# Kernel optimization log

Hardware: AMD Instinct MI355X
Metric: run time of the kernel (lower is better)

Reference implementation:

```python
import jax, jax.numpy as jnp
import numpy as np

B, V, D = 32768, 2, 512   # batch, views (code hard-codes 2 via cat(subject, subject)), hidden dim
S, L = 32, 8              # number of subjects, number of labels -> K = S*L groups
DENS_TEMP = 0.1           # args.Intersubsim_dens_temp (temperature/base_temperature are unused in forward)


def setup_inputs() -> dict:
    key = jax.random.key(0)
    k1, k2, k3 = jax.random.split(key, 3)
    X_data = jax.random.normal(k1, (B, V, D), dtype=jnp.float32)
    subject = jax.random.randint(k2, (B,), 0, S, dtype=jnp.int32)
    labels = jax.random.randint(k3, (B,), 0, L, dtype=jnp.int32)
    return {"X_data": X_data, "subject": subject, "labels": labels}


def reference(X_data, subject, labels):
    K = S * L
    # contrast_feature = cat(unbind(X_data, dim=1), dim=0): view-major stacking -> [V*B, D]
    feat = jnp.concatenate([X_data[:, v, :] for v in range(V)], axis=0)
    sub2 = jnp.concatenate([subject, subject])   # subject_ten
    lab2 = jnp.concatenate([labels, labels])     # labels_ten

    # group id per row; loop order (sorted unique subject, sorted unique label) == s*L + l
    gid = sub2 * L + lab2                         # [2B]
    counts = jax.ops.segment_sum(jnp.ones(gid.shape, feat.dtype), gid, K)   # [K]
    sums = jax.ops.segment_sum(feat, gid, K)                                 # [K, D]
    centroid = sums / counts[:, None]                                        # per-group mean

    # per-point euclidean distance to own-group centroid (torch.cdist)
    dist = jnp.sqrt(jnp.sum((feat - centroid[gid]) ** 2, axis=1))            # [2B]
    # density: mean(dist ** 0.5) / log(n_g + 10) for groups with >1 member
    mean_sqrt = jax.ops.segment_sum(jnp.sqrt(dist), gid, K) / counts
    dens = mean_sqrt / jnp.log(counts + 10.0)
    dmax = jnp.max(jnp.where(counts > 1, dens, -jnp.inf))
    density = jnp.where(counts > 1, dens, dmax)
    density = jnp.clip(density, jnp.quantile(density, 0.1), jnp.quantile(density, 0.9))
    density = DENS_TEMP * density / density.mean()
    # torch path goes through .tolist() -> density carries no gradient
    density = jax.lax.stop_gradient(density)

    # masks: positives = same label, different subject (group index equals raw id here)
    g_sub = jnp.arange(K, dtype=sub2.dtype) // L
    g_lab = jnp.arange(K, dtype=lab2.dtype) % L
    mask = ((sub2[:, None] != g_sub[None, :]) & (lab2[:, None] == g_lab[None, :])).astype(feat.dtype)  # [2B, K]
    # with S>=2 and all labels present, every row has at least one positive -> no row drop

    sim = (feat @ centroid.T) / density[None, :]          # [2B, K]
    sim = sim - jnp.max(sim, axis=1, keepdims=True)
    positive_sim = sim * mask
    # CrossEntropyLoss with soft (unnormalized) float targets: -sum target*log_softmax
    logp = jax.nn.log_softmax(positive_sim, axis=1)
    loss = -jnp.sum(mask * logp, axis=1) / jnp.sum(mask, axis=1)
    return loss.mean()
```

## Files before the change

### kernel.cpp

```cpp
#include <hip/hip_runtime.h>
#include <math.h>

#define BN 32768
#define DN 512
#define SN 32
#define LN 8
#define KN 256
#define N2 65536
#define SPLIT 8

typedef __attribute__((ext_vector_type(8))) short bf16x8;
typedef __attribute__((ext_vector_type(4))) float f32x4;

#define OFF_XBF     0ull
#define OFF_PART    67108864ull
#define OFF_CENTB   71303168ull
#define OFF_PERM    71827456ull
#define OFF_BASE    71958528ull
#define OFF_OFFW    71959556ull
#define OFF_COUNTS  71960580ull
#define OFF_SUMQ    71961604ull
#define OFF_INVD    71962628ull
#define OFF_LOSS    71963652ull
#define OFF_BARS    71963656ull
#define ZERO_OFF    OFF_OFFW
#define ZERO_BYTES  (71963680ull - OFF_OFFW)

__device__ __forceinline__ float atomAddF(float* p, float v) {
  return unsafeAtomicAdd(p, v);
}

__device__ __forceinline__ void gridbar_relaxed(unsigned* cnt, unsigned* flag,
                                                unsigned nblocks) {
  asm volatile("s_waitcnt vmcnt(0)" ::: "memory");
  __syncthreads();
  if (threadIdx.x == 0) {
    unsigned a = __hip_atomic_fetch_add(cnt, 1u, __ATOMIC_RELAXED,
                                        __HIP_MEMORY_SCOPE_AGENT);
    if (a + 1u == nblocks) {
      __hip_atomic_store(flag, 1u, __ATOMIC_RELAXED, __HIP_MEMORY_SCOPE_AGENT);
    } else {
      while (!__hip_atomic_load(flag, __ATOMIC_RELAXED, __HIP_MEMORY_SCOPE_AGENT))
        __builtin_amdgcn_s_sleep(16);
    }
  }
  __syncthreads();
}

__device__ __forceinline__ ushort f2bf(float x) {
  union { float f; unsigned u; } v; v.f = x;
  unsigned u = v.u;
  unsigned r = (u + 0x7fffu + ((u >> 16) & 1u)) >> 16;
  return (ushort)r;
}

__device__ __forceinline__ float bf2f(ushort x) {
  union { unsigned u; float f; } v; v.u = ((unsigned)x) << 16;
  return v.f;
}

__device__ __forceinline__ void async16(const void* g, void* l) {
  __builtin_amdgcn_global_load_lds(
      (const __attribute__((address_space(1))) unsigned int*)g,
      (__attribute__((address_space(3))) unsigned int*)l, 16, 0, 0);
}

__global__ __launch_bounds__(256) void k0_all(const int* __restrict__ subject,
    const int* __restrict__ labels, int* __restrict__ counts, int* __restrict__ base,
    int* __restrict__ offw, int* __restrict__ perm, unsigned* __restrict__ bars) {
  __shared__ int lhist[KN];
  __shared__ int sh[KN];
  __shared__ int lbase[KN];
  const int t = threadIdx.x;
  const int b0 = blockIdx.x * 1024;
  lhist[t] = 0;
  __syncthreads();
  int g[4], lr[4];
#pragma unroll
  for (int k = 0; k < 4; ++k) {
    const int b = b0 + k * 256 + t;
    g[k] = subject[b] * LN + labels[b];
    lr[k] = atomicAdd(&lhist[g[k]], 1);
  }
  __syncthreads();
  const int h = lhist[t];
  if (h) atomicAdd(&counts[t], 2 * h);
  gridbar_relaxed(&bars[0], &bars[1], 32);
  const int rows = ((int)__hip_atomic_load((unsigned*)&counts[t], __ATOMIC_RELAXED,
                                           __HIP_MEMORY_SCOPE_AGENT)) >> 1;
  sh[t] = rows;
  __syncthreads();
  for (int d = 1; d < 256; d <<= 1) {
    int add = (t >= d) ? sh[t - d] : 0;
    __syncthreads();
    sh[t] += add;
    __syncthreads();
  }
  const int excl = sh[t] - rows;
  if (blockIdx.x == 0) {
    base[t] = excl;
    if (t == 255) base[256] = sh[255];
  }
  if (h) lbase[t] = excl + atomicAdd(&offw[t], h);
  __syncthreads();
#pragma unroll
  for (int k = 0; k < 4; ++k)
    perm[lbase[g[k]] + lr[k]] = b0 + k * 256 + t;
}

__global__ __launch_bounds__(256) void k1_sums(const float* __restrict__ X,
    const int* __restrict__ perm, const int* __restrict__ base,
    ushort* __restrict__ Xb, float* __restrict__ partial) {
  __shared__ float buf[4 * 512];
  const int g = blockIdx.x >> 3;
  const int s = blockIdx.x & (SPLIT - 1);
  const int t = threadIdx.x;
  const int w = t >> 6;
  const int lane = t & 63;
  const int start = base[g], end = base[g + 1];
  const int vs = s * 4 + w;

  float4 a0 = {0.f, 0.f, 0.f, 0.f};
  float4 a1 = {0.f, 0.f, 0.f, 0.f};

  int i = start + vs;
  if (i < end) {
    int idx = perm[i];
    const float* bp = X + (size_t)idx * 1024 + lane * 4;
    float4 x0 = *(const float4*)(bp);
    float4 x1 = *(const float4*)(bp + 256);
    float4 x2 = *(const float4*)(bp + 512);
    float4 x3 = *(const float4*)(bp + 768);
    while (true) {
      const int inext = i + 32;
      int idxn = idx;
      float4 y0 = x0, y1 = x1, y2 = x2, y3 = x3;
      if (inext < end) {
        idxn = perm[inext];
        const float* bn = X + (size_t)idxn * 1024 + lane * 4;
        y0 = *(const float4*)(bn);
        y1 = *(const float4*)(bn + 256);
        y2 = *(const float4*)(bn + 512);
        y3 = *(const float4*)(bn + 768);
      }
      a0.x += x0.x + x2.x; a0.y += x0.y + x2.y;
      a0.z += x0.z + x2.z; a0.w += x0.w + x2.w;
      a1.x += x1.x + x3.x; a1.y += x1.y + x3.y;
      a1.z += x1.z + x3.z; a1.w += x1.w + x3.w;
      ushort* xb0 = Xb + (size_t)idx * DN + lane * 4;
      ushort* xb1 = Xb + (size_t)(idx + BN) * DN + lane * 4;
      *(ushort4*)(xb0)       = (ushort4){f2bf(x0.x), f2bf(x0.y), f2bf(x0.z), f2bf(x0.w)};
      *(ushort4*)(xb0 + 256) = (ushort4){f2bf(x1.x), f2bf(x1.y), f2bf(x1.z), f2bf(x1.w)};
      *(ushort4*)(xb1)       = (ushort4){f2bf(x2.x), f2bf(x2.y), f2bf(x2.z), f2bf(x2.w)};
      *(ushort4*)(xb1 + 256) = (ushort4){f2bf(x3.x), f2bf(x3.y), f2bf(x3.z), f2bf(x3.w)};
      if (inext >= end) break;
      i = inext; idx = idxn; x0 = y0; x1 = y1; x2 = y2; x3 = y3;
    }
  }
  *(float4*)&buf[w * 512 + lane * 4] = a0;
  *(float4*)&buf[w * 512 + 256 + lane * 4] = a1;
  __syncthreads();
  if (t < 128) {
    float4 r = {0.f, 0.f, 0.f, 0.f};
#pragma unroll
    for (int ww = 0; ww < 4; ++ww) {
      float4 v = *(float4*)&buf[ww * 512 + t * 4];
      r.x += v.x; r.y += v.y; r.z += v.z; r.w += v.w;
    }
    *(float4*)&partial[((size_t)s * KN + g) * DN + t * 4] = r;
  }
}

__global__ __launch_bounds__(256) void k1b_cent(const float* __restrict__ partial,
    const int* __restrict__ counts, ushort* __restrict__ centB) {
  const int i = blockIdx.x * 256 + threadIdx.x;
  const int g = i >> 9;
  float ss = 0.f;
#pragma unroll
  for (int s = 0; s < SPLIT; ++s) ss += partial[(size_t)s * (KN * DN) + i];
  centB[i] = f2bf(ss / (float)counts[g]);
}

__global__ __launch_bounds__(256) void k3_dist(const ushort* __restrict__ Xb,
    const int* __restrict__ perm, const int* __restrict__ base,
    const ushort* __restrict__ centB, const int* __restrict__ counts,
    float* __restrict__ sumq, float* __restrict__ invd,
    unsigned* __restrict__ bars) {
  __shared__ float wacc[4];
  __shared__ unsigned elect;
  __shared__ float sv[256];
  __shared__ float stv[256];
  const int g = blockIdx.x >> 3;
  const int s = blockIdx.x & (SPLIT - 1);
  const int t = threadIdx.x;
  const int w = t >> 6;
  const int lane = t & 63;
  const int start = base[g], end = base[g + 1];
  const int nviews = 2 * (end - start);
  const ushort* cp = centB + g * DN + lane * 8;
  float cs[8];
#pragma unroll
  for (int k = 0; k < 8; ++k) cs[k] = bf2f(cp[k]);
  float q = 0.f;
  const int vs = s * 4 + w;
  for (int j = vs; j < nviews; j += SPLIT * 4) {
    const int idx = perm[start + (j >> 1)];
    const int row = idx + (j & 1) * BN;
    int4 chunk = *(const int4*)(Xb + (size_t)row * DN + lane * 8);
    const ushort* us = (const ushort*)&chunk;
    float ss = 0.f;
#pragma unroll
    for (int k = 0; k < 8; ++k) {
      float diff = bf2f(us[k]) - cs[k];
      ss += diff * diff;
    }
#pragma unroll
    for (int off = 32; off > 0; off >>= 1) ss += __shfl_down(ss, off, 64);
    if (lane == 0) q += sqrtf(sqrtf(ss));
  }
  if (lane == 0) wacc[w] = q;
  __syncthreads();
  if (t == 0) atomAddF(&sumq[g], wacc[0] + wacc[1] + wacc[2] + wacc[3]);

  asm volatile("s_waitcnt vmcnt(0)" ::: "memory");
  __syncthreads();
  if (t == 0) {
    unsigned a = __hip_atomic_fetch_add(&bars[2], 1u, __ATOMIC_RELAXED,
                                        __HIP_MEMORY_SCOPE_AGENT);
    elect = (a + 1u == (unsigned)(KN * SPLIT)) ? 1u : 0u;
  }
  __syncthreads();
  if (!elect) return;

  const int cnt = counts[t];
  const bool valid = cnt > 1;
  const float sq = __hip_atomic_load(&sumq[t], __ATOMIC_RELAXED,
                                     __HIP_MEMORY_SCOPE_AGENT);
  float dens = 0.f;
  if (valid) dens = (sq / (float)cnt) / logf((float)cnt + 10.f);
  sv[t] = valid ? dens : -INFINITY;
  __syncthreads();
  for (int s2 = 128; s2 > 0; s2 >>= 1) {
    if (t < s2) sv[t] = fmaxf(sv[t], sv[t + s2]);
    __syncthreads();
  }
  const float dmax = sv[0];
  __syncthreads();
  const float d0 = valid ? dens : dmax;
  sv[t] = d0;
  __syncthreads();
  int rank = 0;
  for (int j = 0; j < 256; ++j) {
    float vj = sv[j];
    rank += (vj < d0) || (vj == d0 && j < t);
  }
  stv[rank] = d0;
  __syncthreads();
  const float q10 = 0.5f * (stv[25] + stv[26]);
  const float q90 = 0.5f * (stv[229] + stv[230]);
  const float dc = fminf(fmaxf(d0, q10), q90);
  sv[t] = dc;
  __syncthreads();
  for (int s2 = 128; s2 > 0; s2 >>= 1) {
    if (t < s2) sv[t] += sv[t + s2];
    __syncthreads();
  }
  invd[t] = (sv[0] * (1.0f / 256.f)) / (0.1f * dc);
}

#define TAB (128 * 128)
#define TBB (256 * 128)
__global__ __launch_bounds__(256, 2) void k5_mfma(const ushort* __restrict__ Xb,
    const ushort* __restrict__ centB, const int* __restrict__ subject,
    const int* __restrict__ labels, const float* __restrict__ invd,
    float* __restrict__ losssum, float* __restrict__ out,
    unsigned* __restrict__ bars) {
  __shared__ char smem[TAB + TBB + 1024];
  char* ldsA = smem;
  char* ldsB = smem + TAB;
  float* maxbuf = (float*)smem;
  float* gmax = (float*)(smem + 2048);
  float* ebuf = (float*)(smem + 2560);
  float* zbuf = (float*)(smem + 4608);
  int* labs = (int*)(smem + TAB + TBB);
  int* subs = labs + 128;

  const int t = threadIdx.x;
  const int w = t >> 6;
  const int lane = t & 63;
  const int quad = lane >> 4;
  const int n16 = lane & 15;
  const int li = lane >> 3;
  const int lc = lane & 7;
  const int srcc = lc ^ li;
  const int rowbase = blockIdx.x * 128;

  if (t < 128) {
    int b = (rowbase + t) & (BN - 1);
    labs[t] = labels[b];
    subs[t] = subject[b];
  }

  f32x4 acc[8][4];
#pragma unroll
  for (int mt = 0; mt < 8; ++mt)
#pragma unroll
    for (int nt = 0; nt < 4; ++nt) acc[mt][nt] = (f32x4){0.f, 0.f, 0.f, 0.f};

  const ushort* Arow = Xb + (size_t)rowbase * DN;

  for (int k0 = 0; k0 < DN; k0 += 64) {
    __syncthreads();
#pragma unroll
    for (int q = 0; q < 4; ++q) {
      const int r0 = w * 32 + q * 8;
      async16(Arow + (size_t)(r0 + li) * DN + k0 + srcc * 8, ldsA + r0 * 128);
    }
#pragma unroll
    for (int q = 0; q < 8; ++q) {
      const int g0 = w * 64 + q * 8;
      async16(centB + (size_t)(g0 + li) * DN + k0 + srcc * 8, ldsB + g0 * 128);
    }
    __syncthreads();
#pragma unroll
    for (int s = 0; s < 2; ++s) {
      const int csw = ((s * 4 + quad) ^ (n16 & 7)) * 16;
      bf16x8 bfr[4];
#pragma unroll
      for (int nt = 0; nt < 4; ++nt) {
        int g = w * 64 + nt * 16 + n16;
        bfr[nt] = *(bf16x8*)(ldsB + g * 128 + csw);
      }
#pragma unroll
      for (int mt = 0; mt < 8; ++mt) {
        bf16x8 afr = *(bf16x8*)(ldsA + (mt * 16 + n16) * 128 + csw);
#pragma unroll
        for (int nt = 0; nt < 4; ++nt)
          acc[mt][nt] = __builtin_amdgcn_mfma_f32_16x16x32_bf16(afr, bfr[nt], acc[mt][nt], 0, 0, 0);
      }
    }
  }

  float iv[4];
#pragma unroll
  for (int nt = 0; nt < 4; ++nt) iv[nt] = invd[w * 64 + nt * 16 + n16];

  __syncthreads();

#pragma unroll
  for (int mt = 0; mt < 8; ++mt) {
#pragma unroll
    for (int r = 0; r < 4; ++r) {
      float mm = -INFINITY;
#pragma unroll
      for (int nt = 0; nt < 4; ++nt) mm = fmaxf(mm, acc[mt][nt][r] * iv[nt]);
#pragma unroll
      for (int off = 1; off < 16; off <<= 1) mm = fmaxf(mm, __shfl_xor(mm, off, 64));
      if (n16 == 0) maxbuf[w * 128 + mt * 16 + quad * 4 + r] = mm;
    }
  }
  __syncthreads();
  if (t < 128)
    gmax[t] = fmaxf(fmaxf(maxbuf[t], maxbuf[128 + t]),
                    fmaxf(maxbuf[256 + t], maxbuf[384 + t]));
  __syncthreads();

#pragma unroll
  for (int mt = 0; mt < 8; ++mt) {
#pragma unroll
    for (int r = 0; r < 4; ++r) {
      const int row = mt * 16 + quad * 4 + r;
      const float gm = gmax[row];
      const int lab = labs[row];
      const int sub = subs[row];
      float e = 0.f, z = 0.f;
      if ((n16 & 7) == lab) {
#pragma unroll
        for (int nt = 0; nt < 4; ++nt) {
          int gdiv8 = w * 8 + nt * 2 + (n16 >> 3);
          if (gdiv8 != sub) {
            float svv = acc[mt][nt][r] * iv[nt] - gm;
            e += expf(svv);
            z += svv;
          }
        }
      }
#pragma unroll
      for (int off = 1; off < 16; off <<= 1) {
        e += __shfl_xor(e, off, 64);
        z += __shfl_xor(z, off, 64);
      }
      if (n16 == 0) {
        ebuf[w * 128 + row] = e;
        zbuf[w * 128 + row] = z;
      }
    }
  }
  __syncthreads();

  float lsum = 0.f;
  if (t < 128) {
    float e = ebuf[t] + ebuf[128 + t] + ebuf[256 + t] + ebuf[384 + t];
    float z = zbuf[t] + zbuf[128 + t] + zbuf[256 + t] + zbuf[384 + t];
    lsum = logf(225.f + e) - z * (1.0f / 31.0f);
  }
#pragma unroll
  for (int off = 32; off > 0; off >>= 1) lsum += __shfl_down(lsum, off, 64);
  if (lane == 0 && lsum != 0.f) atomAddF(losssum, lsum);

  asm volatile("s_waitcnt vmcnt(0)" ::: "memory");
  __syncthreads();
  if (t == 0) {
    unsigned a = __hip_atomic_fetch_add(&bars[4], 1u, __ATOMIC_RELAXED,
                                        __HIP_MEMORY_SCOPE_AGENT);
    if (a + 1u == (unsigned)(N2 / 128)) {
      const float ls = __hip_atomic_load(losssum, __ATOMIC_RELAXED,
                                         __HIP_MEMORY_SCOPE_AGENT);
      out[0] = ls * (1.0f / (float)N2);
    }
  }
}

extern "C" void kernel_launch(void* const* d_in, const int* in_sizes, int n_in,
                              void* d_out, int out_size, void* d_ws, size_t ws_size,
                              hipStream_t stream) {
  const float* X = (const float*)d_in[0];
  const int* subject = (const int*)d_in[1];
  const int* labels = (const int*)d_in[2];
  char* ws = (char*)d_ws;
  ushort* Xb = (ushort*)(ws + OFF_XBF);
  float* partial = (float*)(ws + OFF_PART);
  ushort* centB = (ushort*)(ws + OFF_CENTB);
  int* perm = (int*)(ws + OFF_PERM);
  int* basep = (int*)(ws + OFF_BASE);
  int* offw = (int*)(ws + OFF_OFFW);
  int* counts = (int*)(ws + OFF_COUNTS);
  float* sumq = (float*)(ws + OFF_SUMQ);
  float* invd = (float*)(ws + OFF_INVD);
  float* losssum = (float*)(ws + OFF_LOSS);
  unsigned* bars = (unsigned*)(ws + OFF_BARS);

  hipMemsetAsync(ws + ZERO_OFF, 0, ZERO_BYTES, stream);
  k0_all<<<32, 256, 0, stream>>>(subject, labels, counts, basep, offw, perm, bars);
  k1_sums<<<KN * SPLIT, 256, 0, stream>>>(X, perm, basep, Xb, partial);
  k1b_cent<<<(KN * DN) / 256, 256, 0, stream>>>(partial, counts, centB);
  k3_dist<<<KN * SPLIT, 256, 0, stream>>>(Xb, perm, basep, centB, counts,
                                          sumq, invd, bars);
  k5_mfma<<<N2 / 128, 256, 0, stream>>>(Xb, centB, subject, labels, invd,
                                        losssum, (float*)d_out, bars);
}
```

Before: 314.6 us.

## Fuse centroid finalize into distance kernel, widen bf16 stores, halve MFMA row tile

Removes the separate centroid-finalize kernel. Each distance block now reduces the split partial sums for its group into shared memory, and split 0 writes the bf16 centroid. The sums kernel now loads 8 contiguous floats per lane and writes 16-byte bf16 stores instead of 8-byte ones. The MFMA loss kernel uses 64-row tiles with launch bounds of 3 blocks per CU, giving twice as many blocks. The trade-off is redundant partial reads across the 8 split blocks and halved reuse of the centroid tile per block.

```diff
diff --git a/kernel.cpp b/kernel.cpp
--- a/kernel.cpp
+++ b/kernel.cpp
@@ -11,6 +11,7 @@
 
 typedef __attribute__((ext_vector_type(8))) short bf16x8;
 typedef __attribute__((ext_vector_type(4))) float f32x4;
+typedef __attribute__((ext_vector_type(8))) unsigned short ushort8v;
 
 #define OFF_XBF     0ull
 #define OFF_PART    67108864ull
@@ -126,39 +127,40 @@
   int i = start + vs;
   if (i < end) {
     int idx = perm[i];
-    const float* bp = X + (size_t)idx * 1024 + lane * 4;
-    float4 x0 = *(const float4*)(bp);
-    float4 x1 = *(const float4*)(bp + 256);
-    float4 x2 = *(const float4*)(bp + 512);
-    float4 x3 = *(const float4*)(bp + 768);
+    const float* bp = X + (size_t)idx * 1024 + lane * 8;
+    float4 x0  = *(const float4*)(bp);
+    float4 x0b = *(const float4*)(bp + 4);
+    float4 x1  = *(const float4*)(bp + 512);
+    float4 x1b = *(const float4*)(bp + 516);
     while (true) {
       const int inext = i + 32;
       int idxn = idx;
-      float4 y0 = x0, y1 = x1, y2 = x2, y3 = x3;
+      float4 y0 = x0, y0b = x0b, y1 = x1, y1b = x1b;
       if (inext < end) {
         idxn = perm[inext];
-        const float* bn = X + (size_t)idxn * 1024 + lane * 4;
-        y0 = *(const float4*)(bn);
-        y1 = *(const float4*)(bn + 256);
-        y2 = *(const float4*)(bn + 512);
-        y3 = *(const float4*)(bn + 768);
-      }
-      a0.x += x0.x + x2.x; a0.y += x0.y + x2.y;
-      a0.z += x0.z + x2.z; a0.w += x0.w + x2.w;
-      a1.x += x1.x + x3.x; a1.y += x1.y + x3.y;
-      a1.z += x1.z + x3.z; a1.w += x1.w + x3.w;
-      ushort* xb0 = Xb + (size_t)idx * DN + lane * 4;
-      ushort* xb1 = Xb + (size_t)(idx + BN) * DN + lane * 4;
-      *(ushort4*)(xb0)       = (ushort4){f2bf(x0.x), f2bf(x0.y), f2bf(x0.z), f2bf(x0.w)};
-      *(ushort4*)(xb0 + 256) = (ushort4){f2bf(x1.x), f2bf(x1.y), f2bf(x1.z), f2bf(x1.w)};
-      *(ushort4*)(xb1)       = (ushort4){f2bf(x2.x), f2bf(x2.y), f2bf(x2.z), f2bf(x2.w)};
-      *(ushort4*)(xb1 + 256) = (ushort4){f2bf(x3.x), f2bf(x3.y), f2bf(x3.z), f2bf(x3.w)};
+        const float* bn = X + (size_t)idxn * 1024 + lane * 8;
+        y0  = *(const float4*)(bn);
+        y0b = *(const float4*)(bn + 4);
+        y1  = *(const float4*)(bn + 512);
+        y1b = *(const float4*)(bn + 516);
+      }
+      a0.x += x0.x + x1.x;  a0.y += x0.y + x1.y;
+      a0.z += x0.z + x1.z;  a0.w += x0.w + x1.w;
+      a1.x += x0b.x + x1b.x; a1.y += x0b.y + x1b.y;
+      a1.z += x0b.z + x1b.z; a1.w += x0b.w + x1b.w;
+      ushort8v u0, u1;
+      u0[0] = f2bf(x0.x);  u0[1] = f2bf(x0.y);  u0[2] = f2bf(x0.z);  u0[3] = f2bf(x0.w);
+      u0[4] = f2bf(x0b.x); u0[5] = f2bf(x0b.y); u0[6] = f2bf(x0b.z); u0[7] = f2bf(x0b.w);
+      u1[0] = f2bf(x1.x);  u1[1] = f2bf(x1.y);  u1[2] = f2bf(x1.z);  u1[3] = f2bf(x1.w);
+      u1[4] = f2bf(x1b.x); u1[5] = f2bf(x1b.y); u1[6] = f2bf(x1b.z); u1[7] = f2bf(x1b.w);
+      *(ushort8v*)(Xb + (size_t)idx * DN + lane * 8) = u0;
+      *(ushort8v*)(Xb + (size_t)(idx + BN) * DN + lane * 8) = u1;
       if (inext >= end) break;
-      i = inext; idx = idxn; x0 = y0; x1 = y1; x2 = y2; x3 = y3;
-    }
-  }
-  *(float4*)&buf[w * 512 + lane * 4] = a0;
-  *(float4*)&buf[w * 512 + 256 + lane * 4] = a1;
+      i = inext; idx = idxn; x0 = y0; x0b = y0b; x1 = y1; x1b = y1b;
+    }
+  }
+  *(float4*)&buf[w * 512 + lane * 8] = a0;
+  *(float4*)&buf[w * 512 + lane * 8 + 4] = a1;
   __syncthreads();
   if (t < 128) {
     float4 r = {0.f, 0.f, 0.f, 0.f};
@@ -171,21 +173,12 @@
   }
 }
 
-__global__ __launch_bounds__(256) void k1b_cent(const float* __restrict__ partial,
-    const int* __restrict__ counts, ushort* __restrict__ centB) {
-  const int i = blockIdx.x * 256 + threadIdx.x;
-  const int g = i >> 9;
-  float ss = 0.f;
-#pragma unroll
-  for (int s = 0; s < SPLIT; ++s) ss += partial[(size_t)s * (KN * DN) + i];
-  centB[i] = f2bf(ss / (float)counts[g]);
-}
-
 __global__ __launch_bounds__(256) void k3_dist(const ushort* __restrict__ Xb,
     const int* __restrict__ perm, const int* __restrict__ base,
-    const ushort* __restrict__ centB, const int* __restrict__ counts,
-    float* __restrict__ sumq, float* __restrict__ invd,
-    unsigned* __restrict__ bars) {
+    const float* __restrict__ partial, const int* __restrict__ counts,
+    ushort* __restrict__ centB, float* __restrict__ sumq,
+    float* __restrict__ invd, unsigned* __restrict__ bars) {
+  __shared__ float cent[DN];
   __shared__ float wacc[4];
   __shared__ unsigned elect;
   __shared__ float sv[256];
@@ -197,10 +190,26 @@
   const int lane = t & 63;
   const int start = base[g], end = base[g + 1];
   const int nviews = 2 * (end - start);
-  const ushort* cp = centB + g * DN + lane * 8;
+  const int cnt = counts[g];
+  const float invc = 1.0f / (float)cnt;
+
+  float c0 = 0.f, c1 = 0.f;
+#pragma unroll
+  for (int sp = 0; sp < SPLIT; ++sp) {
+    float2 v = *(const float2*)&partial[(size_t)sp * (KN * DN) + g * DN + t * 2];
+    c0 += v.x; c1 += v.y;
+  }
+  c0 *= invc; c1 *= invc;
+  cent[t * 2] = c0; cent[t * 2 + 1] = c1;
+  if (s == 0) {
+    *(ushort2*)&centB[g * DN + t * 2] = (ushort2){f2bf(c0), f2bf(c1)};
+  }
+  __syncthreads();
+
   float cs[8];
 #pragma unroll
-  for (int k = 0; k < 8; ++k) cs[k] = bf2f(cp[k]);
+  for (int k = 0; k < 8; ++k) cs[k] = cent[lane * 8 + k];
+
   float q = 0.f;
   const int vs = s * 4 + w;
   for (int j = vs; j < nviews; j += SPLIT * 4) {
@@ -232,12 +241,12 @@
   __syncthreads();
   if (!elect) return;
 
-  const int cnt = counts[t];
-  const bool valid = cnt > 1;
+  const int cntt = counts[t];
+  const bool valid = cntt > 1;
   const float sq = __hip_atomic_load(&sumq[t], __ATOMIC_RELAXED,
                                      __HIP_MEMORY_SCOPE_AGENT);
   float dens = 0.f;
-  if (valid) dens = (sq / (float)cnt) / logf((float)cnt + 10.f);
+  if (valid) dens = (sq / (float)cntt) / logf((float)cntt + 10.f);
   sv[t] = valid ? dens : -INFINITY;
   __syncthreads();
   for (int s2 = 128; s2 > 0; s2 >>= 1) {
@@ -268,9 +277,9 @@
   invd[t] = (sv[0] * (1.0f / 256.f)) / (0.1f * dc);
 }
 
-#define TAB (128 * 128)
+#define TAB (64 * 128)
 #define TBB (256 * 128)
-__global__ __launch_bounds__(256, 2) void k5_mfma(const ushort* __restrict__ Xb,
+__global__ __launch_bounds__(256, 3) void k5_mfma(const ushort* __restrict__ Xb,
     const ushort* __restrict__ centB, const int* __restrict__ subject,
     const int* __restrict__ labels, const float* __restrict__ invd,
     float* __restrict__ losssum, float* __restrict__ out,
@@ -283,7 +292,7 @@
   float* ebuf = (float*)(smem + 2560);
   float* zbuf = (float*)(smem + 4608);
   int* labs = (int*)(smem + TAB + TBB);
-  int* subs = labs + 128;
+  int* subs = labs + 64;
 
   const int t = threadIdx.x;
   const int w = t >> 6;
@@ -293,17 +302,17 @@
   const int li = lane >> 3;
   const int lc = lane & 7;
   const int srcc = lc ^ li;
-  const int rowbase = blockIdx.x * 128;
-
-  if (t < 128) {
+  const int rowbase = blockIdx.x * 64;
+
+  if (t < 64) {
     int b = (rowbase + t) & (BN - 1);
     labs[t] = labels[b];
     subs[t] = subject[b];
   }
 
-  f32x4 acc[8][4];
-#pragma unroll
-  for (int mt = 0; mt < 8; ++mt)
+  f32x4 acc[4][4];
+#pragma unroll
+  for (int mt = 0; mt < 4; ++mt)
 #pragma unroll
     for (int nt = 0; nt < 4; ++nt) acc[mt][nt] = (f32x4){0.f, 0.f, 0.f, 0.f};
 
@@ -312,8 +321,8 @@
   for (int k0 = 0; k0 < DN; k0 += 64) {
     __syncthreads();
 #pragma unroll
-    for (int q = 0; q < 4; ++q) {
-      const int r0 = w * 32 + q * 8;
+    for (int q = 0; q < 2; ++q) {
+      const int r0 = w * 16 + q * 8;
       async16(Arow + (size_t)(r0 + li) * DN + k0 + srcc * 8, ldsA + r0 * 128);
     }
 #pragma unroll
@@ -332,7 +341,7 @@
         bfr[nt] = *(bf16x8*)(ldsB + g * 128 + csw);
       }
 #pragma unroll
-      for (int mt = 0; mt < 8; ++mt) {
+      for (int mt = 0; mt < 4; ++mt) {
         bf16x8 afr = *(bf16x8*)(ldsA + (mt * 16 + n16) * 128 + csw);
 #pragma unroll
         for (int nt = 0; nt < 4; ++nt)
@@ -348,7 +357,7 @@
   __syncthreads();
 
 #pragma unroll
-  for (int mt = 0; mt < 8; ++mt) {
+  for (int mt = 0; mt < 4; ++mt) {
 #pragma unroll
     for (int r = 0; r < 4; ++r) {
       float mm = -INFINITY;
@@ -356,17 +365,17 @@
       for (int nt = 0; nt < 4; ++nt) mm = fmaxf(mm, acc[mt][nt][r] * iv[nt]);
 #pragma unroll
       for (int off = 1; off < 16; off <<= 1) mm = fmaxf(mm, __shfl_xor(mm, off, 64));
-      if (n16 == 0) maxbuf[w * 128 + mt * 16 + quad * 4 + r] = mm;
-    }
-  }
-  __syncthreads();
-  if (t < 128)
-    gmax[t] = fmaxf(fmaxf(maxbuf[t], maxbuf[128 + t]),
-                    fmaxf(maxbuf[256 + t], maxbuf[384 + t]));
-  __syncthreads();
-
-#pragma unroll
-  for (int mt = 0; mt < 8; ++mt) {
+      if (n16 == 0) maxbuf[w * 64 + mt * 16 + quad * 4 + r] = mm;
+    }
+  }
+  __syncthreads();
+  if (t < 64)
+    gmax[t] = fmaxf(fmaxf(maxbuf[t], maxbuf[64 + t]),
+                    fmaxf(maxbuf[128 + t], maxbuf[192 + t]));
+  __syncthreads();
+
+#pragma unroll
+  for (int mt = 0; mt < 4; ++mt) {
 #pragma unroll
     for (int r = 0; r < 4; ++r) {
       const int row = mt * 16 + quad * 4 + r;
@@ -391,17 +400,17 @@
         z += __shfl_xor(z, off, 64);
       }
       if (n16 == 0) {
-        ebuf[w * 128 + row] = e;
-        zbuf[w * 128 + row] = z;
+        ebuf[w * 64 + row] = e;
+        zbuf[w * 64 + row] = z;
       }
     }
   }
   __syncthreads();
 
   float lsum = 0.f;
-  if (t < 128) {
-    float e = ebuf[t] + ebuf[128 + t] + ebuf[256 + t] + ebuf[384 + t];
-    float z = zbuf[t] + zbuf[128 + t] + zbuf[256 + t] + zbuf[384 + t];
+  if (t < 64) {
+    float e = ebuf[t] + ebuf[64 + t] + ebuf[128 + t] + ebuf[192 + t];
+    float z = zbuf[t] + zbuf[64 + t] + zbuf[128 + t] + zbuf[192 + t];
     lsum = logf(225.f + e) - z * (1.0f / 31.0f);
   }
 #pragma unroll
@@ -413,7 +422,7 @@
   if (t == 0) {
     unsigned a = __hip_atomic_fetch_add(&bars[4], 1u, __ATOMIC_RELAXED,
                                         __HIP_MEMORY_SCOPE_AGENT);
-    if (a + 1u == (unsigned)(N2 / 128)) {
+    if (a + 1u == (unsigned)(N2 / 64)) {
       const float ls = __hip_atomic_load(losssum, __ATOMIC_RELAXED,
                                          __HIP_MEMORY_SCOPE_AGENT);
       out[0] = ls * (1.0f / (float)N2);
@@ -443,9 +452,8 @@
   hipMemsetAsync(ws + ZERO_OFF, 0, ZERO_BYTES, stream);
   k0_all<<<32, 256, 0, stream>>>(subject, labels, counts, basep, offw, perm, bars);
   k1_sums<<<KN * SPLIT, 256, 0, stream>>>(X, perm, basep, Xb, partial);
-  k1b_cent<<<(KN * DN) / 256, 256, 0, stream>>>(partial, counts, centB);
-  k3_dist<<<KN * SPLIT, 256, 0, stream>>>(Xb, perm, basep, centB, counts,
-                                          sumq, invd, bars);
-  k5_mfma<<<N2 / 128, 256, 0, stream>>>(Xb, centB, subject, labels, invd,
-                                        losssum, (float*)d_out, bars);
-}
+  k3_dist<<<KN * SPLIT, 256, 0, stream>>>(Xb, perm, basep, partial, counts,
+                                          centB, sumq, invd, bars);
+  k5_mfma<<<N2 / 64, 256, 0, stream>>>(Xb, centB, subject, labels, invd,
+                                       losssum, (float*)d_out, bars);
+}
```

Result: slower. 323.3 us (+2.8%).

## Double-buffer A tiles in GEMM, read centroids from global, split density kernel

Applied to the files above, without the earlier changes.

The MFMA kernel now double-buffers only the feature (A) tile in LDS and prefetches the next k-slice while computing the current one. The centroid fragments are loaded straight from global memory instead of being staged in LDS, which halves the LDS footprint. Separately, the distance kernel now uses fp32 centroid sums instead of bf16 centroids, and the last-block-elected density tail is moved into its own single-block kernel. The aim is to hide load latency and drop the spin-election overhead, at the cost of uncoalesced global B reads per wave and one extra kernel launch.

```diff
diff --git a/kernel.cpp b/kernel.cpp
--- a/kernel.cpp
+++ b/kernel.cpp
@@ -14,17 +14,18 @@
 
 #define OFF_XBF     0ull
 #define OFF_PART    67108864ull
-#define OFF_CENTB   71303168ull
-#define OFF_PERM    71827456ull
-#define OFF_BASE    71958528ull
-#define OFF_OFFW    71959556ull
-#define OFF_COUNTS  71960580ull
-#define OFF_SUMQ    71961604ull
-#define OFF_INVD    71962628ull
-#define OFF_LOSS    71963652ull
-#define OFF_BARS    71963656ull
+#define OFF_SUMS    71303168ull
+#define OFF_CENTB   71827456ull
+#define OFF_PERM    72089600ull
+#define OFF_BASE    72220672ull
+#define OFF_OFFW    72221700ull
+#define OFF_COUNTS  72222724ull
+#define OFF_SUMQ    72223748ull
+#define OFF_INVD    72224772ull
+#define OFF_LOSS    72225796ull
+#define OFF_BARS    72225800ull
 #define ZERO_OFF    OFF_OFFW
-#define ZERO_BYTES  (71963680ull - OFF_OFFW)
+#define ZERO_BYTES  (72225824ull - OFF_OFFW)
 
 __device__ __forceinline__ float atomAddF(float* p, float v) {
   return unsafeAtomicAdd(p, v);
@@ -172,24 +173,22 @@
 }
 
 __global__ __launch_bounds__(256) void k1b_cent(const float* __restrict__ partial,
-    const int* __restrict__ counts, ushort* __restrict__ centB) {
+    const int* __restrict__ counts, float* __restrict__ sums,
+    ushort* __restrict__ centB) {
   const int i = blockIdx.x * 256 + threadIdx.x;
   const int g = i >> 9;
   float ss = 0.f;
 #pragma unroll
   for (int s = 0; s < SPLIT; ++s) ss += partial[(size_t)s * (KN * DN) + i];
+  sums[i] = ss;
   centB[i] = f2bf(ss / (float)counts[g]);
 }
 
 __global__ __launch_bounds__(256) void k3_dist(const ushort* __restrict__ Xb,
     const int* __restrict__ perm, const int* __restrict__ base,
-    const ushort* __restrict__ centB, const int* __restrict__ counts,
-    float* __restrict__ sumq, float* __restrict__ invd,
-    unsigned* __restrict__ bars) {
+    const float* __restrict__ sums, const int* __restrict__ counts,
+    float* __restrict__ sumq) {
   __shared__ float wacc[4];
-  __shared__ unsigned elect;
-  __shared__ float sv[256];
-  __shared__ float stv[256];
   const int g = blockIdx.x >> 3;
   const int s = blockIdx.x & (SPLIT - 1);
   const int t = threadIdx.x;
@@ -197,10 +196,12 @@
   const int lane = t & 63;
   const int start = base[g], end = base[g + 1];
   const int nviews = 2 * (end - start);
-  const ushort* cp = centB + g * DN + lane * 8;
-  float cs[8];
-#pragma unroll
-  for (int k = 0; k < 8; ++k) cs[k] = bf2f(cp[k]);
+  const float invc = 1.0f / (float)counts[g];
+  const float* sp = sums + g * DN + lane * 8;
+  float4 c0 = *(const float4*)sp;
+  float4 c1 = *(const float4*)(sp + 4);
+  const float cs[8] = {c0.x * invc, c0.y * invc, c0.z * invc, c0.w * invc,
+                       c1.x * invc, c1.y * invc, c1.z * invc, c1.w * invc};
   float q = 0.f;
   const int vs = s * 4 + w;
   for (int j = vs; j < nviews; j += SPLIT * 4) {
@@ -221,27 +222,21 @@
   if (lane == 0) wacc[w] = q;
   __syncthreads();
   if (t == 0) atomAddF(&sumq[g], wacc[0] + wacc[1] + wacc[2] + wacc[3]);
-
-  asm volatile("s_waitcnt vmcnt(0)" ::: "memory");
-  __syncthreads();
-  if (t == 0) {
-    unsigned a = __hip_atomic_fetch_add(&bars[2], 1u, __ATOMIC_RELAXED,
-                                        __HIP_MEMORY_SCOPE_AGENT);
-    elect = (a + 1u == (unsigned)(KN * SPLIT)) ? 1u : 0u;
-  }
-  __syncthreads();
-  if (!elect) return;
-
+}
+
+__global__ __launch_bounds__(256) void k4_density(const float* __restrict__ sumq,
+    const int* __restrict__ counts, float* __restrict__ invd) {
+  __shared__ float sv[256];
+  __shared__ float st[256];
+  const int t = threadIdx.x;
   const int cnt = counts[t];
   const bool valid = cnt > 1;
-  const float sq = __hip_atomic_load(&sumq[t], __ATOMIC_RELAXED,
-                                     __HIP_MEMORY_SCOPE_AGENT);
   float dens = 0.f;
-  if (valid) dens = (sq / (float)cnt) / logf((float)cnt + 10.f);
+  if (valid) dens = (sumq[t] / (float)cnt) / logf((float)cnt + 10.f);
   sv[t] = valid ? dens : -INFINITY;
   __syncthreads();
-  for (int s2 = 128; s2 > 0; s2 >>= 1) {
-    if (t < s2) sv[t] = fmaxf(sv[t], sv[t + s2]);
+  for (int s = 128; s > 0; s >>= 1) {
+    if (t < s) sv[t] = fmaxf(sv[t], sv[t + s]);
     __syncthreads();
   }
   const float dmax = sv[0];
@@ -254,35 +249,33 @@
     float vj = sv[j];
     rank += (vj < d0) || (vj == d0 && j < t);
   }
-  stv[rank] = d0;
-  __syncthreads();
-  const float q10 = 0.5f * (stv[25] + stv[26]);
-  const float q90 = 0.5f * (stv[229] + stv[230]);
+  st[rank] = d0;
+  __syncthreads();
+  const float q10 = 0.5f * (st[25] + st[26]);
+  const float q90 = 0.5f * (st[229] + st[230]);
   const float dc = fminf(fmaxf(d0, q10), q90);
   sv[t] = dc;
   __syncthreads();
-  for (int s2 = 128; s2 > 0; s2 >>= 1) {
-    if (t < s2) sv[t] += sv[t + s2];
+  for (int s = 128; s > 0; s >>= 1) {
+    if (t < s) sv[t] += sv[t + s];
     __syncthreads();
   }
-  invd[t] = (sv[0] * (1.0f / 256.f)) / (0.1f * dc);
+  const float mean = sv[0] * (1.0f / 256.f);
+  invd[t] = mean / (0.1f * dc);
 }
 
 #define TAB (128 * 128)
-#define TBB (256 * 128)
 __global__ __launch_bounds__(256, 2) void k5_mfma(const ushort* __restrict__ Xb,
     const ushort* __restrict__ centB, const int* __restrict__ subject,
     const int* __restrict__ labels, const float* __restrict__ invd,
     float* __restrict__ losssum, float* __restrict__ out,
     unsigned* __restrict__ bars) {
-  __shared__ char smem[TAB + TBB + 1024];
-  char* ldsA = smem;
-  char* ldsB = smem + TAB;
+  __shared__ char smem[2 * TAB + 1024];
   float* maxbuf = (float*)smem;
   float* gmax = (float*)(smem + 2048);
   float* ebuf = (float*)(smem + 2560);
   float* zbuf = (float*)(smem + 4608);
-  int* labs = (int*)(smem + TAB + TBB);
+  int* labs = (int*)(smem + 2 * TAB);
   int* subs = labs + 128;
 
   const int t = threadIdx.x;
@@ -309,43 +302,48 @@
 
   const ushort* Arow = Xb + (size_t)rowbase * DN;
 
+#pragma unroll
+  for (int q = 0; q < 4; ++q) {
+    const int r0 = w * 32 + q * 8;
+    async16(Arow + (size_t)(r0 + li) * DN + srcc * 8, smem + r0 * 128);
+  }
+  __syncthreads();
+
+  int ab = 0;
   for (int k0 = 0; k0 < DN; k0 += 64) {
-    __syncthreads();
-#pragma unroll
-    for (int q = 0; q < 4; ++q) {
-      const int r0 = w * 32 + q * 8;
-      async16(Arow + (size_t)(r0 + li) * DN + k0 + srcc * 8, ldsA + r0 * 128);
-    }
-#pragma unroll
-    for (int q = 0; q < 8; ++q) {
-      const int g0 = w * 64 + q * 8;
-      async16(centB + (size_t)(g0 + li) * DN + k0 + srcc * 8, ldsB + g0 * 128);
-    }
-    __syncthreads();
+    if (k0 + 64 < DN) {
+#pragma unroll
+      for (int q = 0; q < 4; ++q) {
+        const int r0 = w * 32 + q * 8;
+        async16(Arow + (size_t)(r0 + li) * DN + (k0 + 64) + srcc * 8,
+                smem + (ab ^ TAB) + r0 * 128);
+      }
+    }
 #pragma unroll
     for (int s = 0; s < 2; ++s) {
-      const int csw = ((s * 4 + quad) ^ (n16 & 7)) * 16;
+      const int chunk = s * 4 + quad;
+      const int csw = (chunk ^ (n16 & 7)) * 16;
       bf16x8 bfr[4];
 #pragma unroll
       for (int nt = 0; nt < 4; ++nt) {
-        int g = w * 64 + nt * 16 + n16;
-        bfr[nt] = *(bf16x8*)(ldsB + g * 128 + csw);
+        const int g = w * 64 + nt * 16 + n16;
+        bfr[nt] = *(const bf16x8*)(centB + (size_t)g * DN + k0 + chunk * 8);
       }
 #pragma unroll
       for (int mt = 0; mt < 8; ++mt) {
-        bf16x8 afr = *(bf16x8*)(ldsA + (mt * 16 + n16) * 128 + csw);
+        bf16x8 afr = *(bf16x8*)(smem + ab + (mt * 16 + n16) * 128 + csw);
 #pragma unroll
         for (int nt = 0; nt < 4; ++nt)
           acc[mt][nt] = __builtin_amdgcn_mfma_f32_16x16x32_bf16(afr, bfr[nt], acc[mt][nt], 0, 0, 0);
       }
     }
+    __syncthreads();
+    ab ^= TAB;
   }
 
   float iv[4];
 #pragma unroll
   for (int nt = 0; nt < 4; ++nt) iv[nt] = invd[w * 64 + nt * 16 + n16];
-
-  __syncthreads();
 
 #pragma unroll
   for (int mt = 0; mt < 8; ++mt) {
@@ -430,6 +428,7 @@
   char* ws = (char*)d_ws;
   ushort* Xb = (ushort*)(ws + OFF_XBF);
   float* partial = (float*)(ws + OFF_PART);
+  float* sums = (float*)(ws + OFF_SUMS);
   ushort* centB = (ushort*)(ws + OFF_CENTB);
   int* perm = (int*)(ws + OFF_PERM);
   int* basep = (int*)(ws + OFF_BASE);
@@ -443,9 +442,9 @@
   hipMemsetAsync(ws + ZERO_OFF, 0, ZERO_BYTES, stream);
   k0_all<<<32, 256, 0, stream>>>(subject, labels, counts, basep, offw, perm, bars);
   k1_sums<<<KN * SPLIT, 256, 0, stream>>>(X, perm, basep, Xb, partial);
-  k1b_cent<<<(KN * DN) / 256, 256, 0, stream>>>(partial, counts, centB);
-  k3_dist<<<KN * SPLIT, 256, 0, stream>>>(Xb, perm, basep, centB, counts,
-                                          sumq, invd, bars);
+  k1b_cent<<<(KN * DN) / 256, 256, 0, stream>>>(partial, counts, sums, centB);
+  k3_dist<<<KN * SPLIT, 256, 0, stream>>>(Xb, perm, basep, sums, counts, sumq);
+  k4_density<<<1, 256, 0, stream>>>(sumq, counts, invd);
   k5_mfma<<<N2 / 128, 256, 0, stream>>>(Xb, centB, subject, labels, invd,
                                         losssum, (float*)d_out, bars);
 }
```

Result: faster. 304.1 us (-3.3%).
